# Kernel optimization log

Hardware: AMD Instinct MI355X
Metric: run time of the kernel (lower is better)

The kernel has to match this reference:

```python
import jax, jax.numpy as jnp
import numpy as np

B, C, H, W = 32, 1536, 14, 14   # input is (B*4, C, H, W); joint -> (B, C, 2H, 2W)
CI = C // 2                     # non-local inter_channels
EPS = 1e-5


def conv1x1(x, w, b):
    # x: (b, cin, h, w); w: (cout, cin); b: (cout,)
    return jnp.einsum('bchw,oc->bohw', x, w) + b[None, :, None, None]


def maxpool2(x):
    b, c, h, w = x.shape
    return x.reshape(b, c, h // 2, 2, w // 2, 2).max(axis=(3, 5))


def setup_inputs():
    key = jax.random.key(0)
    ks = jax.random.split(key, 12)
    s = 0.02
    return {
        'x': jax.random.normal(ks[0], (B * 4, C, H, W), jnp.float32),
        'w_theta': jax.random.normal(ks[1], (CI, C), jnp.float32) * s,
        'b_theta': jnp.zeros((CI,), jnp.float32),
        'w_phi': jax.random.normal(ks[2], (CI, C), jnp.float32) * s,
        'b_phi': jnp.zeros((CI,), jnp.float32),
        'w_g': jax.random.normal(ks[3], (CI, C), jnp.float32) * s,
        'b_g': jnp.zeros((CI,), jnp.float32),
        'w_W': jax.random.normal(ks[4], (C, CI), jnp.float32) * s,
        'b_W': jnp.zeros((C,), jnp.float32),
        'bn_gamma': jax.random.normal(ks[5], (C,), jnp.float32) * 0.1 + 1.0,
        'bn_beta': jax.random.normal(ks[6], (C,), jnp.float32) * 0.1,
        'bn_mean': jax.random.normal(ks[7], (C,), jnp.float32) * 0.1,
        'bn_var': jnp.ones((C,), jnp.float32),
    }


def joint(x):
    # (B*4, C, H, W) -> (B, C, 2H, 2W): 4 views tiled in a 2x2 grid
    x4 = x.reshape(B, 4, C, H, W)
    top = jnp.concatenate([x4[:, 0], x4[:, 1]], axis=-1)   # (B, C, H, 2W)
    bot = jnp.concatenate([x4[:, 2], x4[:, 3]], axis=-1)
    return jnp.concatenate([top, bot], axis=-2)             # (B, C, 2H, 2W)


def reference(x, w_theta, b_theta, w_phi, b_phi, w_g, b_g, w_W, b_W,
              bn_gamma, bn_beta, bn_mean, bn_var):
    xj = joint(x)                                           # (B, C, Hj, Wj)
    b, c, hj, wj = xj.shape
    n = hj * wj                                             # 784 query positions

    theta = conv1x1(xj, w_theta, b_theta).reshape(b, CI, n)             # (B, CI, N)
    phi = maxpool2(conv1x1(xj, w_phi, b_phi)).reshape(b, CI, -1)        # (B, CI, N/4)
    g = maxpool2(conv1x1(xj, w_g, b_g)).reshape(b, CI, -1)              # (B, CI, N/4)

    f = jnp.einsum('bcn,bcm->bnm', theta, phi)              # (B, N, N/4)
    attn = jax.nn.softmax(f, axis=-1)
    y = jnp.einsum('bnm,bcm->bcn', attn, g)                 # (B, CI, N)
    y = y.reshape(b, CI, hj, wj)

    w_y = conv1x1(y, w_W, b_W)
    # BatchNorm (inference form)
    inv = jax.lax.rsqrt(bn_var + EPS)
    w_y = (w_y - bn_mean[None, :, None, None]) * (bn_gamma * inv)[None, :, None, None] \
          + bn_beta[None, :, None, None]
    return w_y + xj
```

## Files before the change

kernel.cpp:

```cpp
#include <hip/hip_runtime.h>
#include <hip/hip_bf16.h>

typedef __attribute__((ext_vector_type(8))) _Float16 f16x8;
typedef __attribute__((ext_vector_type(4))) float f32x4;
typedef __attribute__((ext_vector_type(4))) unsigned short us4;
typedef __attribute__((ext_vector_type(8))) unsigned short us8;

#define B_   32
#define C_   1536
#define CI_  768
#define N_   784
#define S_   196
#define MP_  224
#define MK_  196

__device__ __forceinline__ unsigned short f2h(float f) {
    _Float16 h = (_Float16)f;
    return __builtin_bit_cast(unsigned short, h);
}
__device__ __forceinline__ f32x4 mfma_f16(f16x8 a, f16x8 b, f32x4 c) {
    return __builtin_amdgcn_mfma_f32_16x16x32_f16(a, b, c, 0, 0, 0);
}
__device__ __forceinline__ void gl_lds16(const unsigned short* g, unsigned short* l) {
    __builtin_amdgcn_global_load_lds(
        (const __attribute__((address_space(1))) unsigned int*)g,
        (__attribute__((address_space(3))) unsigned int*)l, 16, 0, 0);
}

__device__ __forceinline__ void stage23(const unsigned short* Arow,
                                        const unsigned short* Brow,
                                        unsigned short* A_s, unsigned short* B_s,
                                        int k0, int stride,
                                        int wv, int l4r, int l4c_sw) {
    for (int c = wv; c < 23; c += 4) {
        if (c < 16) {
            gl_lds16(Arow + (size_t)(c * 16 + l4r) * stride + k0 + l4c_sw * 8,
                     A_s + c * 512);
        } else {
            int cb = c - 16;
            gl_lds16(Brow + (size_t)(cb * 16 + l4r) * stride + k0 + l4c_sw * 8,
                     B_s + cb * 512);
        }
    }
}

__global__ __launch_bounds__(256) void k_cvt(const float* __restrict__ src,
                                             unsigned short* __restrict__ dst,
                                             int count4) {
    int idx = blockIdx.x * 256 + threadIdx.x;
    if (idx < count4) {
        f32x4 v = ((const f32x4*)src)[idx];
        us4 o;
        o[0] = f2h(v[0]); o[1] = f2h(v[1]); o[2] = f2h(v[2]); o[3] = f2h(v[3]);
        ((us4*)dst)[idx] = o;
    }
}

__global__ __launch_bounds__(256) void k_build_xjT(const float* __restrict__ x,
                                                   unsigned short* __restrict__ xjT) {
    __shared__ __align__(16) unsigned short lds[196 * 40];
    int c0 = blockIdx.x * 32;
    int b4 = blockIdx.y;
    int b = b4 >> 2, v = b4 & 3;
    int tid = threadIdx.x;
    const float* src = x + ((size_t)b4 * C_ + c0) * S_;
    for (int idx = tid; idx < 32 * 49; idx += 256) {
        int cl = idx / 49;
        int sq = idx - cl * 49;
        f32x4 val = *(const f32x4*)(src + (size_t)cl * S_ + sq * 4);
        int s = sq * 4;
        lds[(s + 0) * 40 + cl] = f2h(val[0]);
        lds[(s + 1) * 40 + cl] = f2h(val[1]);
        lds[(s + 2) * 40 + cl] = f2h(val[2]);
        lds[(s + 3) * 40 + cl] = f2h(val[3]);
    }
    __syncthreads();
    int rowbase = (v >> 1) * 14, colbase = (v & 1) * 14;
    for (int idx = tid; idx < 196 * 4; idx += 256) {
        int s = idx >> 2, ch = idx & 3;
        int hh = s / 14, ww = s - hh * 14;
        int n = (rowbase + hh) * 28 + colbase + ww;
        us8 val = *(const us8*)(&lds[s * 40 + ch * 8]);
        *(us8*)(xjT + ((size_t)b * N_ + n) * C_ + c0 + ch * 8) = val;
    }
}

__global__ __launch_bounds__(256) void k_bnprep(const float* __restrict__ bw,
                                                const float* __restrict__ gamma,
                                                const float* __restrict__ beta,
                                                const float* __restrict__ mean,
                                                const float* __restrict__ var,
                                                float* __restrict__ scale,
                                                float* __restrict__ shift) {
    int i = blockIdx.x * 256 + threadIdx.x;
    if (i < C_) {
        float sc = gamma[i] * rsqrtf(var[i] + 1e-5f);
        scale[i] = sc;
        shift[i] = (bw[i] - mean[i]) * sc + beta[i];
    }
}

#define COMPUTE_STEP4(As, Bs)                                                     \
    {                                                                             \
        f16x8 a0_ = *(const f16x8*)(&(As)[((wv * 4 + 0) * 16 + lr) * 32 + rcol]); \
        f16x8 a1_ = *(const f16x8*)(&(As)[((wv * 4 + 1) * 16 + lr) * 32 + rcol]); \
        f16x8 a2_ = *(const f16x8*)(&(As)[((wv * 4 + 2) * 16 + lr) * 32 + rcol]); \
        f16x8 a3_ = *(const f16x8*)(&(As)[((wv * 4 + 3) * 16 + lr) * 32 + rcol]); \
        _Pragma("unroll")                                                         \
        for (int j = 0; j < 7; ++j) {                                             \
            f16x8 bb = *(const f16x8*)(&(Bs)[(j * 16 + lr) * 32 + rcol]);         \
            acc[0][j] = mfma_f16(a0_, bb, acc[0][j]);                             \
            acc[1][j] = mfma_f16(a1_, bb, acc[1][j]);                             \
            acc[2][j] = mfma_f16(a2_, bb, acc[2][j]);                             \
            acc[3][j] = mfma_f16(a3_, bb, acc[3][j]);                             \
        }                                                                         \
    }

__global__ __launch_bounds__(256, 3) void k_conv3(
    const unsigned short* __restrict__ xjT,
    const unsigned short* __restrict__ wf,
    const float* __restrict__ b_theta, const float* __restrict__ b_phi,
    const float* __restrict__ b_g,
    unsigned short* __restrict__ theta_T, unsigned short* __restrict__ phi_p,
    unsigned short* __restrict__ g_p) {
    __shared__ __align__(16) unsigned char smem[47104];
    unsigned short* A0 = (unsigned short*)smem;
    unsigned short* B0 = A0 + 8192;
    unsigned short* A1 = A0 + 11776;
    unsigned short* B1 = A0 + 19968;
    float* fLDS = (float*)smem;

    int tn = blockIdx.x;
    int tm = blockIdx.y;
    int b  = blockIdx.z;
    int o0 = tm * 256, n0 = tn * 112;
    int region = o0 / 768;
    int obase = o0 - region * 768;
    const float* bias = (region == 0) ? b_theta : (region == 1) ? b_phi : b_g;

    int tid = threadIdx.x;
    int wv = tid >> 6, lane = tid & 63, lr = lane & 15, quad = lane >> 4;
    int l4r = lane >> 2, l4c = lane & 3;
    int l4c_sw = l4c ^ ((l4r >> 1) & 3);
    int rcol = (quad ^ ((lr >> 1) & 3)) * 8;

    f32x4 acc[4][7];
#pragma unroll
    for (int i = 0; i < 4; ++i)
#pragma unroll
        for (int j = 0; j < 7; ++j) acc[i][j] = (f32x4){0.f, 0.f, 0.f, 0.f};

    const unsigned short* Arow = wf + (size_t)o0 * C_;
    const unsigned short* Brow = xjT + ((size_t)b * N_ + n0) * C_;

    stage23(Arow, Brow, A0, B0, 0, C_, wv, l4r, l4c_sw);
    __syncthreads();
    for (int kk = 0; kk < 48; kk += 2) {
        stage23(Arow, Brow, A1, B1, (kk + 1) * 32, C_, wv, l4r, l4c_sw);
        COMPUTE_STEP4(A0, B0);
        __syncthreads();
        if (kk + 2 < 48)
            stage23(Arow, Brow, A0, B0, (kk + 2) * 32, C_, wv, l4r, l4c_sw);
        COMPUTE_STEP4(A1, B1);
        __syncthreads();
    }

    for (int h = 0; h < 4; ++h) {
        if (wv == h) {
#pragma unroll
            for (int i = 0; i < 4; ++i)
#pragma unroll
                for (int j = 0; j < 7; ++j)
#pragma unroll
                    for (int r = 0; r < 4; ++r) {
                        int o_rel = i * 16 + quad * 4 + r;
                        int n_l = j * 16 + lr;
                        fLDS[o_rel * 112 + n_l] = acc[i][j][r];
                    }
        }
        __syncthreads();
        if (region == 0) {
            for (int idx = tid; idx < 112 * 8; idx += 256) {
                int n_l = idx >> 3, ch = idx & 7;
                us8 outv;
#pragma unroll
                for (int k = 0; k < 8; ++k) {
                    int o_rel = ch * 8 + k;
                    float val = fLDS[o_rel * 112 + n_l] + bias[obase + h * 64 + o_rel];
                    outv[k] = f2h(val);
                }
                *(us8*)(theta_T + ((size_t)b * N_ + n0 + n_l) * CI_ + o0 + h * 64 + ch * 8) = outv;
            }
        } else if (region == 1) {
            for (int idx = tid; idx < 28 * 8; idx += 256) {
                int mm = idx >> 3, ch = idx & 7;
                int a = mm / 14, mw = mm - a * 14;
                int m = (tn * 2 + a) * 14 + mw;
                int sb = a * 56 + mw * 2;
                us8 outv;
#pragma unroll
                for (int k = 0; k < 8; ++k) {
                    int o_rel = ch * 8 + k;
                    const float* p = &fLDS[o_rel * 112 + sb];
                    float val = fmaxf(fmaxf(p[0], p[1]), fmaxf(p[28], p[29]));
                    val += bias[obase + h * 64 + o_rel];
                    outv[k] = f2h(val);
                }
                *(us8*)(phi_p + ((size_t)b * MP_ + m) * CI_ + obase + h * 64 + ch * 8) = outv;
            }
        } else {
            for (int idx = tid; idx < 128; idx += 256) {
                int o_rel = idx >> 1, a = idx & 1;
                int ci = obase + h * 64 + o_rel;
                unsigned short* dst = g_p + ((size_t)b * CI_ + ci) * MP_ + (tn * 2 + a) * 14;
                const float* p0 = &fLDS[o_rel * 112 + a * 56];
                float bv = bias[obase + h * 64 + o_rel];
#pragma unroll
                for (int mw = 0; mw < 14; ++mw) {
                    const float* p = p0 + mw * 2;
                    dst[mw] = f2h(fmaxf(fmaxf(p[0], p[1]), fmaxf(p[28], p[29])) + bv);
                }
            }
        }
        __syncthreads();
    }
}

__global__ __launch_bounds__(256) void k_attn(
    const unsigned short* __restrict__ theta_T,
    const unsigned short* __restrict__ phi_p,
    const unsigned short* __restrict__ g_p,
    unsigned short* __restrict__ y) {
    __shared__ __align__(16) float f_s[32 * 228];

    int nb = blockIdx.x, b = blockIdx.y;
    int n0 = nb * 32;
    int tid = threadIdx.x, wv = tid >> 6, lane = tid & 63, lr = lane & 15, quad = lane >> 4;
    int mf0 = wv * 4;
    int nm = (mf0 + 4 <= 14) ? 4 : (14 - mf0);

    int na0 = n0 + lr;       if (na0 > 783) na0 = 783;
    int na1 = n0 + 16 + lr;  if (na1 > 783) na1 = 783;
    const unsigned short* tA0 = theta_T + ((size_t)b * N_ + na0) * CI_ + quad * 8;
    const unsigned short* tA1 = theta_T + ((size_t)b * N_ + na1) * CI_ + quad * 8;

    f32x4 acc[2][4];
#pragma unroll
    for (int i = 0; i < 2; ++i)
#pragma unroll
        for (int j = 0; j < 4; ++j) acc[i][j] = (f32x4){0.f, 0.f, 0.f, 0.f};

    for (int kk = 0; kk < 24; ++kk) {
        int k0 = kk * 32;
        f16x8 a0 = *(const f16x8*)(tA0 + k0);
        f16x8 a1 = *(const f16x8*)(tA1 + k0);
        for (int j = 0; j < nm; ++j) {
            f16x8 bb = *(const f16x8*)(phi_p +
                ((size_t)b * MP_ + (mf0 + j) * 16 + lr) * CI_ + k0 + quad * 8);
            acc[0][j] = mfma_f16(a0, bb, acc[0][j]);
            acc[1][j] = mfma_f16(a1, bb, acc[1][j]);
        }
    }
    for (int i = 0; i < 2; ++i)
        for (int j = 0; j < nm; ++j)
#pragma unroll
            for (int r = 0; r < 4; ++r)
                f_s[(i * 16 + quad * 4 + r) * 228 + (mf0 + j) * 16 + lr] = acc[i][j][r];
    __syncthreads();
    {
        int row = tid >> 3, sub = tid & 7;
        float* rowp = f_s + row * 228;
        int m0 = sub * 28;
        float mx = -1e30f;
#pragma unroll
        for (int m = 0; m < 28; ++m)
            if (m0 + m < MK_) mx = fmaxf(mx, rowp[m0 + m]);
        mx = fmaxf(mx, __shfl_xor(mx, 1));
        mx = fmaxf(mx, __shfl_xor(mx, 2));
        mx = fmaxf(mx, __shfl_xor(mx, 4));
        float sum = 0.f;
#pragma unroll
        for (int m = 0; m < 28; ++m) {
            float e = (m0 + m < MK_) ? __expf(rowp[m0 + m] - mx) : 0.f;
            rowp[m0 + m] = e;
            sum += e;
        }
        sum += __shfl_xor(sum, 1);
        sum += __shfl_xor(sum, 2);
        sum += __shfl_xor(sum, 4);
        float inv = 1.0f / sum;
#pragma unroll
        for (int m = 0; m < 28; ++m) rowp[m0 + m] *= inv;
    }
    __syncthreads();
    for (int c3 = 0; c3 < 3; ++c3) {
        int ci0 = c3 * 256;
        f32x4 acc2[2][4];
#pragma unroll
        for (int i = 0; i < 2; ++i)
#pragma unroll
            for (int j = 0; j < 4; ++j) acc2[i][j] = (f32x4){0.f, 0.f, 0.f, 0.f};
        for (int km = 0; km < 7; ++km) {
            int k0 = km * 32;
            f16x8 a[2];
#pragma unroll
            for (int i = 0; i < 2; ++i) {
                const float* fp = &f_s[(i * 16 + lr) * 228 + k0 + quad * 8];
                f16x8 t;
#pragma unroll
                for (int j = 0; j < 8; ++j) t[j] = (_Float16)fp[j];
                a[i] = t;
            }
#pragma unroll
            for (int j = 0; j < 4; ++j) {
                f16x8 bb = *(const f16x8*)(g_p +
                    ((size_t)b * CI_ + ci0 + (wv * 4 + j) * 16 + lr) * MP_ + k0 + quad * 8);
                acc2[0][j] = mfma_f16(a[0], bb, acc2[0][j]);
                acc2[1][j] = mfma_f16(a[1], bb, acc2[1][j]);
            }
        }
#pragma unroll
        for (int i = 0; i < 2; ++i)
#pragma unroll
            for (int j = 0; j < 4; ++j)
#pragma unroll
                for (int r = 0; r < 4; ++r) {
                    int n = n0 + i * 16 + quad * 4 + r;
                    if (n < N_) {
                        int ci = ci0 + (wv * 4 + j) * 16 + lr;
                        y[((size_t)b * N_ + n) * CI_ + ci] = f2h(acc2[i][j][r]);
                    }
                }
    }
}

__global__ __launch_bounds__(256, 3) void k_final(
    const unsigned short* __restrict__ yb,
    const unsigned short* __restrict__ wfW,
    const float* __restrict__ scale, const float* __restrict__ shift,
    const float* __restrict__ x,
    float* __restrict__ out) {
    __shared__ __align__(16) unsigned short smem_us[23552];
    unsigned short* A0 = smem_us;
    unsigned short* B0 = smem_us + 8192;
    unsigned short* A1 = smem_us + 11776;
    unsigned short* B1 = smem_us + 19968;
    int tn = blockIdx.x, tm = blockIdx.y, b = blockIdx.z;
    int o0 = tm * 256, n0 = tn * 112;
    int tid = threadIdx.x, wv = tid >> 6, lane = tid & 63, lr = lane & 15, quad = lane >> 4;
    int l4r = lane >> 2, l4c = lane & 3;
    int l4c_sw = l4c ^ ((l4r >> 1) & 3);
    int rcol = (quad ^ ((lr >> 1) & 3)) * 8;

    f32x4 acc[4][7];
#pragma unroll
    for (int i = 0; i < 4; ++i)
#pragma unroll
        for (int j = 0; j < 7; ++j) acc[i][j] = (f32x4){0.f, 0.f, 0.f, 0.f};

    const unsigned short* Arow = wfW + (size_t)o0 * CI_;
    const unsigned short* Brow = yb + ((size_t)b * N_ + n0) * CI_;

    stage23(Arow, Brow, A0, B0, 0, CI_, wv, l4r, l4c_sw);
    __syncthreads();
    for (int kk = 0; kk < 24; kk += 2) {
        stage23(Arow, Brow, A1, B1, (kk + 1) * 32, CI_, wv, l4r, l4c_sw);
        COMPUTE_STEP4(A0, B0);
        __syncthreads();
        if (kk + 2 < 24)
            stage23(Arow, Brow, A0, B0, (kk + 2) * 32, CI_, wv, l4r, l4c_sw);
        COMPUTE_STEP4(A1, B1);
        __syncthreads();
    }
#pragma unroll
    for (int i = 0; i < 4; ++i)
#pragma unroll
        for (int r = 0; r < 4; ++r) {
            int o = o0 + (wv * 4 + i) * 16 + quad * 4 + r;
            float sc = scale[o], sh = shift[o];
#pragma unroll
            for (int j = 0; j < 7; ++j) {
                int n = n0 + j * 16 + lr;
                int hh = n / 28, ww = n - hh * 28;
                int vv = ((hh >= 14) ? 2 : 0) + ((ww >= 14) ? 1 : 0);
                int s = (hh - ((hh >= 14) ? 14 : 0)) * 14 + (ww - ((ww >= 14) ? 14 : 0));
                float xval = x[((size_t)(b * 4 + vv) * C_ + o) * S_ + s];
                out[((size_t)b * C_ + o) * N_ + n] = acc[i][j][r] * sc + sh + xval;
            }
        }
}

extern "C" void kernel_launch(void* const* d_in, const int* in_sizes, int n_in,
                              void* d_out, int out_size, void* d_ws, size_t ws_size,
                              hipStream_t stream) {
    (void)in_sizes; (void)n_in; (void)out_size; (void)ws_size;
    const float* x       = (const float*)d_in[0];
    const float* w_theta = (const float*)d_in[1];
    const float* b_theta = (const float*)d_in[2];
    const float* w_phi   = (const float*)d_in[3];
    const float* b_phi   = (const float*)d_in[4];
    const float* w_g     = (const float*)d_in[5];
    const float* b_g     = (const float*)d_in[6];
    const float* w_W     = (const float*)d_in[7];
    const float* b_W     = (const float*)d_in[8];
    const float* gamma   = (const float*)d_in[9];
    const float* beta    = (const float*)d_in[10];
    const float* mean    = (const float*)d_in[11];
    const float* var     = (const float*)d_in[12];

    char* ob = (char*)d_out;
    unsigned short* xjT     = (unsigned short*)(ob);
    unsigned short* theta_T = (unsigned short*)(ob + 77070336);
    unsigned short* phi_p   = (unsigned short*)(ob + 115605504);
    unsigned short* g_p     = (unsigned short*)(ob + 126615552);
    unsigned short* wf3     = (unsigned short*)(ob + 137625600);

    char* ws = (char*)d_ws;
    unsigned short* yb    = (unsigned short*)(ws);
    unsigned short* wfW   = (unsigned short*)(ws + 38535168);
    float*          scale = (float*)(ws + 40894464);
    float*          shift = (float*)(ws + 40900608);

    hipMemsetAsync(phi_p, 0, 11010048, stream);
    hipMemsetAsync(g_p, 0, 11010048, stream);

    k_bnprep<<<6, 256, 0, stream>>>(b_W, gamma, beta, mean, var, scale, shift);
    k_cvt<<<1152, 256, 0, stream>>>(w_theta, wf3,                294912);
    k_cvt<<<1152, 256, 0, stream>>>(w_phi,   wf3 + 768 * 1536,   294912);
    k_cvt<<<1152, 256, 0, stream>>>(w_g,     wf3 + 2 * 768 * 1536, 294912);
    k_cvt<<<1152, 256, 0, stream>>>(w_W,     wfW,                294912);
    k_build_xjT<<<dim3(48, 128), 256, 0, stream>>>(x, xjT);
    k_conv3<<<dim3(7, 9, 32), 256, 0, stream>>>(xjT, wf3, b_theta, b_phi, b_g,
                                                theta_T, phi_p, g_p);
    k_attn<<<dim3(25, 32), 256, 0, stream>>>(theta_T, phi_p, g_p, yb);
    k_final<<<dim3(7, 6, 32), 256, 0, stream>>>(yb, wfW, scale, shift, x,
                                                (float*)d_out);
}
```

Baseline: 849.2 us.

## Triple-buffer GEMM K-loop with vmcnt-based waits and MFMA priority

```diff
diff --git a/kernel.cpp b/kernel.cpp
--- a/kernel.cpp
+++ b/kernel.cpp
@@ -27,12 +27,12 @@
         (__attribute__((address_space(3))) unsigned int*)l, 16, 0, 0);
 }
 
-__device__ __forceinline__ void stage23(const unsigned short* Arow,
+__device__ __forceinline__ void stage24(const unsigned short* Arow,
                                         const unsigned short* Brow,
                                         unsigned short* A_s, unsigned short* B_s,
                                         int k0, int stride,
                                         int wv, int l4r, int l4c_sw) {
-    for (int c = wv; c < 23; c += 4) {
+    for (int c = wv; c < 24; c += 4) {
         if (c < 16) {
             gl_lds16(Arow + (size_t)(c * 16 + l4r) * stride + k0 + l4c_sw * 8,
                      A_s + c * 512);
@@ -43,6 +43,13 @@
         }
     }
 }
+
+#define PIPE_WAIT_BARRIER()                                   \
+    do {                                                      \
+        asm volatile("s_waitcnt vmcnt(6)" ::: "memory");      \
+        __builtin_amdgcn_s_barrier();                         \
+        __builtin_amdgcn_sched_barrier(0);                    \
+    } while (0)
 
 __global__ __launch_bounds__(256) void k_cvt(const float* __restrict__ src,
                                              unsigned short* __restrict__ dst,
@@ -102,6 +109,7 @@
 
 #define COMPUTE_STEP4(As, Bs)                                                     \
     {                                                                             \
+        __builtin_amdgcn_s_setprio(1);                                            \
         f16x8 a0_ = *(const f16x8*)(&(As)[((wv * 4 + 0) * 16 + lr) * 32 + rcol]); \
         f16x8 a1_ = *(const f16x8*)(&(As)[((wv * 4 + 1) * 16 + lr) * 32 + rcol]); \
         f16x8 a2_ = *(const f16x8*)(&(As)[((wv * 4 + 2) * 16 + lr) * 32 + rcol]); \
@@ -114,20 +122,23 @@
             acc[2][j] = mfma_f16(a2_, bb, acc[2][j]);                             \
             acc[3][j] = mfma_f16(a3_, bb, acc[3][j]);                             \
         }                                                                         \
-    }
-
-__global__ __launch_bounds__(256, 3) void k_conv3(
+        __builtin_amdgcn_s_setprio(0);                                            \
+    }
+
+__global__ __launch_bounds__(256, 2) void k_conv3(
     const unsigned short* __restrict__ xjT,
     const unsigned short* __restrict__ wf,
     const float* __restrict__ b_theta, const float* __restrict__ b_phi,
     const float* __restrict__ b_g,
     unsigned short* __restrict__ theta_T, unsigned short* __restrict__ phi_p,
     unsigned short* __restrict__ g_p) {
-    __shared__ __align__(16) unsigned char smem[47104];
+    __shared__ __align__(16) unsigned char smem[73728];
     unsigned short* A0 = (unsigned short*)smem;
     unsigned short* B0 = A0 + 8192;
-    unsigned short* A1 = A0 + 11776;
-    unsigned short* B1 = A0 + 19968;
+    unsigned short* A1 = A0 + 12288;
+    unsigned short* B1 = A0 + 20480;
+    unsigned short* A2 = A0 + 24576;
+    unsigned short* B2 = A0 + 32768;
     float* fLDS = (float*)smem;
 
     int tn = blockIdx.x;
@@ -153,17 +164,21 @@
     const unsigned short* Arow = wf + (size_t)o0 * C_;
     const unsigned short* Brow = xjT + ((size_t)b * N_ + n0) * C_;
 
-    stage23(Arow, Brow, A0, B0, 0, C_, wv, l4r, l4c_sw);
+    stage24(Arow, Brow, A0, B0, 0, C_, wv, l4r, l4c_sw);
+    stage24(Arow, Brow, A1, B1, 32, C_, wv, l4r, l4c_sw);
+    for (int kk = 0; kk < 48; kk += 3) {
+        PIPE_WAIT_BARRIER();
+        stage24(Arow, Brow, A2, B2, (kk + 2 < 48 ? kk + 2 : 47) * 32, C_, wv, l4r, l4c_sw);
+        COMPUTE_STEP4(A0, B0);
+        PIPE_WAIT_BARRIER();
+        stage24(Arow, Brow, A0, B0, (kk + 3 < 48 ? kk + 3 : 47) * 32, C_, wv, l4r, l4c_sw);
+        COMPUTE_STEP4(A1, B1);
+        PIPE_WAIT_BARRIER();
+        stage24(Arow, Brow, A1, B1, (kk + 4 < 48 ? kk + 4 : 47) * 32, C_, wv, l4r, l4c_sw);
+        COMPUTE_STEP4(A2, B2);
+    }
+    asm volatile("s_waitcnt vmcnt(0)" ::: "memory");
     __syncthreads();
-    for (int kk = 0; kk < 48; kk += 2) {
-        stage23(Arow, Brow, A1, B1, (kk + 1) * 32, C_, wv, l4r, l4c_sw);
-        COMPUTE_STEP4(A0, B0);
-        __syncthreads();
-        if (kk + 2 < 48)
-            stage23(Arow, Brow, A0, B0, (kk + 2) * 32, C_, wv, l4r, l4c_sw);
-        COMPUTE_STEP4(A1, B1);
-        __syncthreads();
-    }
 
     for (int h = 0; h < 4; ++h) {
         if (wv == h) {
@@ -334,17 +349,19 @@
     }
 }
 
-__global__ __launch_bounds__(256, 3) void k_final(
+__global__ __launch_bounds__(256, 2) void k_final(
     const unsigned short* __restrict__ yb,
     const unsigned short* __restrict__ wfW,
     const float* __restrict__ scale, const float* __restrict__ shift,
     const float* __restrict__ x,
     float* __restrict__ out) {
-    __shared__ __align__(16) unsigned short smem_us[23552];
+    __shared__ __align__(16) unsigned short smem_us[36864];
     unsigned short* A0 = smem_us;
     unsigned short* B0 = smem_us + 8192;
-    unsigned short* A1 = smem_us + 11776;
-    unsigned short* B1 = smem_us + 19968;
+    unsigned short* A1 = smem_us + 12288;
+    unsigned short* B1 = smem_us + 20480;
+    unsigned short* A2 = smem_us + 24576;
+    unsigned short* B2 = smem_us + 32768;
     int tn = blockIdx.x, tm = blockIdx.y, b = blockIdx.z;
     int o0 = tm * 256, n0 = tn * 112;
     int tid = threadIdx.x, wv = tid >> 6, lane = tid & 63, lr = lane & 15, quad = lane >> 4;
@@ -361,17 +378,21 @@
     const unsigned short* Arow = wfW + (size_t)o0 * CI_;
     const unsigned short* Brow = yb + ((size_t)b * N_ + n0) * CI_;
 
-    stage23(Arow, Brow, A0, B0, 0, CI_, wv, l4r, l4c_sw);
+    stage24(Arow, Brow, A0, B0, 0, CI_, wv, l4r, l4c_sw);
+    stage24(Arow, Brow, A1, B1, 32, CI_, wv, l4r, l4c_sw);
+    for (int kk = 0; kk < 24; kk += 3) {
+        PIPE_WAIT_BARRIER();
+        stage24(Arow, Brow, A2, B2, (kk + 2 < 24 ? kk + 2 : 23) * 32, CI_, wv, l4r, l4c_sw);
+        COMPUTE_STEP4(A0, B0);
+        PIPE_WAIT_BARRIER();
+        stage24(Arow, Brow, A0, B0, (kk + 3 < 24 ? kk + 3 : 23) * 32, CI_, wv, l4r, l4c_sw);
+        COMPUTE_STEP4(A1, B1);
+        PIPE_WAIT_BARRIER();
+        stage24(Arow, Brow, A1, B1, (kk + 4 < 24 ? kk + 4 : 23) * 32, CI_, wv, l4r, l4c_sw);
+        COMPUTE_STEP4(A2, B2);
+    }
+    asm volatile("s_waitcnt vmcnt(0)" ::: "memory");
     __syncthreads();
-    for (int kk = 0; kk < 24; kk += 2) {
-        stage23(Arow, Brow, A1, B1, (kk + 1) * 32, CI_, wv, l4r, l4c_sw);
-        COMPUTE_STEP4(A0, B0);
-        __syncthreads();
-        if (kk + 2 < 24)
-            stage23(Arow, Brow, A0, B0, (kk + 2) * 32, CI_, wv, l4r, l4c_sw);
-        COMPUTE_STEP4(A1, B1);
-        __syncthreads();
-    }
 #pragma unroll
     for (int i = 0; i < 4; ++i)
 #pragma unroll
```

Result: faster. 796.7 us (-6.2%).
